# Kernel tuning notes

Hardware: AMD Instinct MI355X
Metric: run time of the kernel (lower is better)

Reference implementation:

```python
import jax, jax.numpy as jnp
import numpy as np

D_MODEL, D_STATE, D_CONV, D_INNER, DT_RANK = 1024, 16, 4, 2048, 64
BATCH, LENGTH = 4, 2048


def setup_inputs() -> dict:
    key = jax.random.key(0)
    ks = jax.random.split(key, 10)
    dt_init_std = DT_RANK ** -0.5
    # dt_proj bias init: inverse-softplus of dt sampled log-uniform in [dt_min, dt_max]
    dt_min, dt_max, dt_floor = 0.001, 0.1, 1e-4
    u = jax.random.uniform(ks[9], (D_INNER,))
    dt = jnp.clip(jnp.exp(u * (np.log(dt_max) - np.log(dt_min)) + np.log(dt_min)), dt_floor, None)
    b_dt = dt + jnp.log(-jnp.expm1(-dt))
    return {
        "x": jax.random.normal(ks[0], (BATCH, LENGTH, D_MODEL), jnp.float32),
        "W_in": jax.random.normal(ks[1], (2 * D_INNER, D_MODEL), jnp.float32) * D_MODEL ** -0.5,
        "conv_w": jax.random.normal(ks[2], (D_INNER, 1, D_CONV), jnp.float32) * D_CONV ** -0.5,
        "conv_b": jax.random.normal(ks[3], (D_INNER,), jnp.float32) * 0.01,
        "W_x": jax.random.normal(ks[4], (DT_RANK + 2 * D_STATE, D_INNER), jnp.float32) * D_INNER ** -0.5,
        "W_dt": jax.random.uniform(ks[5], (D_INNER, DT_RANK), jnp.float32, -dt_init_std, dt_init_std),
        "b_dt": b_dt.astype(jnp.float32),
        "A_raw": jax.random.normal(ks[6], (D_STATE, D_INNER), jnp.float32),
        "D": jax.random.normal(ks[7], (D_INNER,), jnp.float32),
        "W_out": jax.random.normal(ks[8], (D_MODEL, D_INNER), jnp.float32) * D_INNER ** -0.5,
    }


def _mamba_fwd(x, W_in, conv_w, conv_b, W_x, W_dt, b_dt, A_raw, D, W_out):
    b, l, _ = x.shape
    d_inner = W_in.shape[0] // 2
    d_state = A_raw.shape[0]
    dt_rank = W_dt.shape[1]
    xz = jnp.einsum('bld,ed->ble', x, W_in)            # (b, l, 2*d_inner)
    xc, z = jnp.split(xz, 2, axis=-1)
    # causal depthwise conv (torch pads both sides by d_conv-1 then keeps first l == left pad)
    xc = xc.transpose(0, 2, 1)                          # (b, d, l)
    k = conv_w.shape[-1]
    xc = jax.lax.conv_general_dilated(
        xc, conv_w, (1,), [(k - 1, 0)],
        dimension_numbers=('NCH', 'OIH', 'NCH'),
        feature_group_count=d_inner) + conv_b[None, :, None]
    xc = jax.nn.silu(xc).transpose(0, 2, 1)             # (b, l, d)
    dbc = jnp.einsum('bld,ed->ble', xc, W_x)            # (b, l, dt_rank+2*d_state)
    dt, B, C = jnp.split(dbc, [dt_rank, dt_rank + d_state], axis=-1)
    delta = jax.nn.softplus(jnp.einsum('blr,dr->bld', dt, W_dt) + b_dt)  # (b, l, d)
    A = -jnp.exp(A_raw)                                 # (n, d), negative real

    def step(h, inp):
        x_t, dlt, B_t, C_t = inp                        # (b,d),(b,d),(b,n),(b,n)
        dA = jnp.exp(dlt[:, None, :] * A[None])          # (b, n, d)
        h = dA * h + (dlt[:, None, :] * B_t[:, :, None]) * x_t[:, None, :]
        y_t = jnp.einsum('bn,bnd->bd', C_t, h) + D * x_t
        return h, y_t

    h0 = jnp.zeros((b, d_state, d_inner), x.dtype)
    xs = (xc.transpose(1, 0, 2), delta.transpose(1, 0, 2),
          B.transpose(1, 0, 2), C.transpose(1, 0, 2))
    _, ys = jax.lax.scan(step, h0, xs)                  # (l, b, d)
    y = ys.transpose(1, 0, 2) * jax.nn.silu(z)
    return jnp.einsum('bld,md->blm', y, W_out)


def reference(x, W_in, conv_w, conv_b, W_x, W_dt, b_dt, A_raw, D, W_out):
    return _mamba_fwd(x, W_in, conv_w, conv_b, W_x, W_dt, b_dt, A_raw, D, W_out)
```

## Files before the change

### kernel.cpp

```cpp
#include <hip/hip_runtime.h>
#include <hip/hip_bf16.h>

typedef __bf16 bf16;
typedef __bf16 bf16x4 __attribute__((ext_vector_type(4)));
typedef __bf16 bf16x8 __attribute__((ext_vector_type(8)));
typedef float f32x4 __attribute__((ext_vector_type(4)));

__device__ __forceinline__ float fast_exp2(float x) {
#if __has_builtin(__builtin_amdgcn_exp2f)
    return __builtin_amdgcn_exp2f(x);
#else
    return exp2f(x);
#endif
}

__device__ __forceinline__ float fast_log(float x) {
#if __has_builtin(__builtin_amdgcn_logf)
    return __builtin_amdgcn_logf(x) * 0.6931471805599453f;
#else
    return __logf(x);
#endif
}

__device__ __forceinline__ void gload16(bf16* lds, const bf16* g) {
    __builtin_amdgcn_global_load_lds(
        (const __attribute__((address_space(1))) void*)g,
        (__attribute__((address_space(3))) void*)lds,
        16, 0, 0);
}

__device__ __forceinline__ bf16x8 cvt8(const float* p) {
    float4 a = *(const float4*)p;
    float4 b = *(const float4*)(p + 4);
    bf16x8 r;
    r[0] = (bf16)a.x; r[1] = (bf16)a.y; r[2] = (bf16)a.z; r[3] = (bf16)a.w;
    r[4] = (bf16)b.x; r[5] = (bf16)b.y; r[6] = (bf16)b.z; r[7] = (bf16)b.w;
    return r;
}

__global__ __launch_bounds__(256) void cvt_bf16(
    const float* __restrict__ in, bf16* __restrict__ out, int n8)
{
    int i = blockIdx.x * 256 + threadIdx.x;
    if (i < n8)
        *(bf16x8*)(out + (size_t)i * 8) = cvt8(in + (size_t)i * 8);
}

template <int EPI, typename TC>
__global__ __launch_bounds__(256, 2) void gemm_bt(
    const bf16* __restrict__ A, int lda,
    const bf16* __restrict__ B, int ldb,
    TC* __restrict__ C, int ldc,
    int K, int Neff, const float* __restrict__ bias,
    const bf16* __restrict__ gmul, size_t zstride)
{
    __shared__ bf16 As[128 * 32];
    __shared__ bf16 Bs[128 * 32];

    const int tid  = threadIdx.x;
    const int lane = tid & 63;
    const int wave = tid >> 6;
    const int quad = lane >> 4;
    const int l16  = lane & 15;
    const int wm   = (wave >> 1) << 6;
    const int wn   = (wave & 1) << 6;
    const int bm   = blockIdx.x << 7;
    const int bn   = blockIdx.y << 7;
    const int kb   = blockIdx.z * K;

    const int srow = (wave << 4) + (lane >> 2);
    const int scol = (lane & 3) << 3;

    const bf16* Ag0 = A + (size_t)(bm + srow) * lda + kb + scol;
    const bf16* Ag1 = Ag0 + (size_t)lda * 64;
    int br0 = bn + srow;      br0 = br0 < Neff ? br0 : Neff - 1;
    int br1 = bn + srow + 64; br1 = br1 < Neff ? br1 : Neff - 1;
    const bf16* Bg0 = B + (size_t)br0 * ldb + kb + scol;
    const bf16* Bg1 = B + (size_t)br1 * ldb + kb + scol;

    bf16* Asd0 = As + wave * 512;
    bf16* Asd1 = As + wave * 512 + 2048;
    bf16* Bsd0 = Bs + wave * 512;
    bf16* Bsd1 = Bs + wave * 512 + 2048;

    f32x4 acc[4][4] = {};

    for (int k0 = 0; k0 < K; k0 += 32) {
        if (k0) __syncthreads();
        gload16(Asd0, Ag0 + k0);
        gload16(Asd1, Ag1 + k0);
        gload16(Bsd0, Bg0 + k0);
        gload16(Bsd1, Bg1 + k0);
        __syncthreads();

        bf16x8 af[4], bfr[4];
#pragma unroll
        for (int i = 0; i < 4; ++i) {
            af[i]  = *(const bf16x8*)(As + (wm + i * 16 + l16) * 32 + quad * 8);
            bfr[i] = *(const bf16x8*)(Bs + (wn + i * 16 + l16) * 32 + quad * 8);
        }
#pragma unroll
        for (int mi = 0; mi < 4; ++mi)
#pragma unroll
            for (int ni = 0; ni < 4; ++ni)
                acc[mi][ni] = __builtin_amdgcn_mfma_f32_16x16x32_bf16(
                    af[mi], bfr[ni], acc[mi][ni], 0, 0, 0);
    }

    TC* Cz = C + (size_t)blockIdx.z * zstride;

#pragma unroll
    for (int mi = 0; mi < 4; ++mi) {
        const int row = bm + wm + mi * 16 + quad * 4;
#pragma unroll
        for (int ni = 0; ni < 4; ++ni) {
            const int col = bn + wn + ni * 16 + l16;
            if (col < Neff) {
                float bc = (EPI == 1) ? bias[col] : 0.f;
#pragma unroll
                for (int r = 0; r < 4; ++r) {
                    float v = acc[mi][ni][r];
                    if (EPI == 1) {
                        v += bc;
                        float sp = fast_log(1.f + __expf(v));
                        v = (v > 15.f) ? v : sp;
                    } else if (EPI == 2) {
                        float g = v / (1.f + __expf(-v));
                        v = (float)gmul[(size_t)(row + r) * ldc + col] * g;
                    }
                    Cz[(size_t)(row + r) * ldc + col] = (TC)v;
                }
            }
        }
    }
}

__global__ __launch_bounds__(256) void reduce_dbc(
    const float* __restrict__ P, bf16* __restrict__ dbc)
{
    const size_t i = ((size_t)blockIdx.x * 256 + threadIdx.x) * 4;
    f32x4 s = *(const f32x4*)(P + i);
#pragma unroll
    for (int z = 1; z < 4; ++z) {
        f32x4 p = *(const f32x4*)(P + (size_t)z * 786432 + i);
        s[0] += p[0]; s[1] += p[1]; s[2] += p[2]; s[3] += p[3];
    }
    bf16x4 o;
    o[0] = (bf16)s[0]; o[1] = (bf16)s[1]; o[2] = (bf16)s[2]; o[3] = (bf16)s[3];
    *(bf16x4*)(dbc + i) = o;
}

__global__ __launch_bounds__(256) void conv_kernel(
    const bf16* __restrict__ xh, const float* __restrict__ cw,
    const float* __restrict__ cb, bf16* __restrict__ xc)
{
    const int t0 = blockIdx.x << 3;
    const int b  = blockIdx.y;
    const int d  = threadIdx.x * 8;

    float4 wv[8];
#pragma unroll
    for (int i = 0; i < 8; ++i)
        wv[i] = *(const float4*)(cw + (d + i) * 4);

    float4 cb0 = *(const float4*)(cb + d);
    float4 cb1 = *(const float4*)(cb + d + 4);

    float acc[8][8];
#pragma unroll
    for (int k = 0; k < 8; ++k) {
        acc[k][0] = cb0.x; acc[k][1] = cb0.y; acc[k][2] = cb0.z; acc[k][3] = cb0.w;
        acc[k][4] = cb1.x; acc[k][5] = cb1.y; acc[k][6] = cb1.z; acc[k][7] = cb1.w;
    }

    const bf16* base = xh + ((size_t)b * 2048 + t0) * 2048 + d;

#pragma unroll
    for (int r = 0; r < 11; ++r) {
        const int t_in = t0 - 3 + r;
        if (t_in >= 0) {
            bf16x8 v = *(const bf16x8*)(base + (size_t)(r - 3) * 2048);
            float vf[8];
#pragma unroll
            for (int i = 0; i < 8; ++i) vf[i] = (float)v[i];
#pragma unroll
            for (int j = 0; j < 4; ++j) {
                const int local = r - j;
                if (local >= 0 && local < 8) {
#pragma unroll
                    for (int i = 0; i < 8; ++i) {
                        float w = (j == 0) ? wv[i].x : (j == 1) ? wv[i].y
                                : (j == 2) ? wv[i].z : wv[i].w;
                        acc[local][i] += w * vf[i];
                    }
                }
            }
        }
    }

    bf16* ob = xc + ((size_t)b * 2048 + t0) * 2048 + d;
#pragma unroll
    for (int k = 0; k < 8; ++k) {
        bf16x8 o;
#pragma unroll
        for (int i = 0; i < 8; ++i) {
            float s = acc[k][i];
            o[i] = (bf16)(s / (1.f + __expf(-s)));
        }
        *(bf16x8*)(ob + (size_t)k * 2048) = o;
    }
}

__global__ __launch_bounds__(256, 4) void scan_p1(
    const bf16* __restrict__ delta, const bf16* __restrict__ dbc,
    const float* __restrict__ A_raw, const bf16* __restrict__ xc,
    float* __restrict__ Hbuf, bf16* __restrict__ Abuf)
{
    const int d = (blockIdx.x << 8) + threadIdx.x;
    const int b = blockIdx.y;
    const int c = blockIdx.z;

    float A2[16];
#pragma unroll
    for (int n = 0; n < 16; ++n)
        A2[n] = -__expf(A_raw[n * 2048 + d]) * 1.44269504f;

    float h[16];
#pragma unroll
    for (int n = 0; n < 16; ++n) h[n] = 0.f;
    float sdt = 0.f;

    const size_t xbase = ((size_t)(b * 2048 + c * 64)) * 2048 + d;
    const bf16* xp = xc + xbase;
    const bf16* dp = delta + xbase;
    const bf16* bp = dbc + ((size_t)(b * 2048 + c * 64)) * 96 + 64;

    bf16 xr = xp[0], dr = dp[0];
    bf16x8 B0 = *(const bf16x8*)(bp);
    bf16x8 B1 = *(const bf16x8*)(bp + 8);

#pragma unroll 4
    for (int t = 0; t < 64; ++t) {
        const float x  = (float)xr;
        const float dt = (float)dr;
        const bf16x8 Bl = B0, Bh = B1;
        if (t < 63) {
            xr = xp[(size_t)(t + 1) * 2048];
            dr = dp[(size_t)(t + 1) * 2048];
            const bf16* nb = bp + (size_t)(t + 1) * 96;
            B0 = *(const bf16x8*)nb;
            B1 = *(const bf16x8*)(nb + 8);
        }
        const float dx = dt * x;
        sdt += dt;
#pragma unroll
        for (int n = 0; n < 8; ++n) {
            float e = fast_exp2(dt * A2[n]);
            h[n] = e * h[n] + (float)Bl[n] * dx;
        }
#pragma unroll
        for (int n = 0; n < 8; ++n) {
            float e = fast_exp2(dt * A2[n + 8]);
            h[n + 8] = e * h[n + 8] + (float)Bh[n] * dx;
        }
    }

    const size_t hbase = (((size_t)b * 32 + c) * 2048 + d) * 16;
    f32x4* Hp = (f32x4*)(Hbuf + hbase);
#pragma unroll
    for (int r = 0; r < 4; ++r) {
        f32x4 v;
        v[0] = h[r * 4]; v[1] = h[r * 4 + 1];
        v[2] = h[r * 4 + 2]; v[3] = h[r * 4 + 3];
        Hp[r] = v;
    }
    bf16x8 a0, a1;
#pragma unroll
    for (int n = 0; n < 8; ++n) {
        a0[n] = (bf16)fast_exp2(A2[n] * sdt);
        a1[n] = (bf16)fast_exp2(A2[n + 8] * sdt);
    }
    *(bf16x8*)(Abuf + hbase) = a0;
    *(bf16x8*)(Abuf + hbase + 8) = a1;
}

__global__ __launch_bounds__(256) void scan_p2(
    float* __restrict__ Hbuf, const bf16* __restrict__ Abuf)
{
    const int id  = blockIdx.x * 256 + threadIdx.x;
    const int b   = id >> 15;
    const int rem = id & 32767;
    const size_t base = (size_t)b * 32 * 32768 + rem;

    float Hv[32]; bf16 Av[32];
#pragma unroll
    for (int c = 0; c < 32; ++c) {
        Hv[c] = Hbuf[base + (size_t)c * 32768];
        Av[c] = Abuf[base + (size_t)c * 32768];
    }
    float ht = Hv[0];
#pragma unroll
    for (int c = 1; c < 32; ++c) {
        ht = Hv[c] + (float)Av[c] * ht;
        Hbuf[base + (size_t)c * 32768] = ht;
    }
}

__global__ __launch_bounds__(256, 4) void scan_p3(
    const bf16* __restrict__ delta, const bf16* __restrict__ dbc,
    const float* __restrict__ A_raw, const float* __restrict__ Dvec,
    const float* __restrict__ Hbuf, const bf16* xc, bf16* ry)
{
    const int d = (blockIdx.x << 8) + threadIdx.x;
    const int b = blockIdx.y;
    const int c = blockIdx.z;

    float A2[16];
#pragma unroll
    for (int n = 0; n < 16; ++n)
        A2[n] = -__expf(A_raw[n * 2048 + d]) * 1.44269504f;
    const float Dd = Dvec[d];

    float h[16];
    if (c > 0) {
        const f32x4* Hp = (const f32x4*)(
            Hbuf + (((size_t)b * 32 + (c - 1)) * 2048 + d) * 16);
#pragma unroll
        for (int r = 0; r < 4; ++r) {
            f32x4 v = Hp[r];
            h[r * 4] = v[0]; h[r * 4 + 1] = v[1];
            h[r * 4 + 2] = v[2]; h[r * 4 + 3] = v[3];
        }
    } else {
#pragma unroll
        for (int n = 0; n < 16; ++n) h[n] = 0.f;
    }

    const size_t xbase = ((size_t)(b * 2048 + c * 64)) * 2048 + d;
    const bf16* xp = xc + xbase;
    const bf16* dp = delta + xbase;
    const bf16* bp = dbc + ((size_t)(b * 2048 + c * 64)) * 96 + 64;
    bf16* yp = ry + xbase;

    bf16 xr = xp[0], dr = dp[0];
    bf16x8 B0 = *(const bf16x8*)(bp);
    bf16x8 B1 = *(const bf16x8*)(bp + 8);
    bf16x8 C0 = *(const bf16x8*)(bp + 16);
    bf16x8 C1 = *(const bf16x8*)(bp + 24);

#pragma unroll 4
    for (int t = 0; t < 64; ++t) {
        const float x  = (float)xr;
        const float dt = (float)dr;
        const bf16x8 Bl = B0, Bh = B1, Cl = C0, Ch = C1;
        if (t < 63) {
            xr = xp[(size_t)(t + 1) * 2048];
            dr = dp[(size_t)(t + 1) * 2048];
            const bf16* nb = bp + (size_t)(t + 1) * 96;
            B0 = *(const bf16x8*)nb;
            B1 = *(const bf16x8*)(nb + 8);
            C0 = *(const bf16x8*)(nb + 16);
            C1 = *(const bf16x8*)(nb + 24);
        }
        const float dx = dt * x;
        float y = Dd * x;
#pragma unroll
        for (int n = 0; n < 8; ++n) {
            float e = fast_exp2(dt * A2[n]);
            h[n] = e * h[n] + (float)Bl[n] * dx;
            y += (float)Cl[n] * h[n];
        }
#pragma unroll
        for (int n = 0; n < 8; ++n) {
            float e = fast_exp2(dt * A2[n + 8]);
            h[n + 8] = e * h[n + 8] + (float)Bh[n] * dx;
            y += (float)Ch[n] * h[n + 8];
        }
        yp[(size_t)t * 2048] = (bf16)y;
    }
}

extern "C" void kernel_launch(void* const* d_in, const int* in_sizes, int n_in,
                              void* d_out, int out_size, void* d_ws, size_t ws_size,
                              hipStream_t stream)
{
    const float* x      = (const float*)d_in[0];
    const float* W_in   = (const float*)d_in[1];
    const float* conv_w = (const float*)d_in[2];
    const float* conv_b = (const float*)d_in[3];
    const float* W_x    = (const float*)d_in[4];
    const float* W_dt   = (const float*)d_in[5];
    const float* b_dt   = (const float*)d_in[6];
    const float* A_raw  = (const float*)d_in[7];
    const float* Dvec   = (const float*)d_in[8];
    const float* W_out  = (const float*)d_in[9];
    float* out = (float*)d_out;

    char* ws = (char*)d_ws;
    bf16*  buf0   = (bf16*)(ws + 0);
    bf16*  buf1   = (bf16*)(ws + 33554432);
    char*  dob    = (char*)d_out;
    bf16*  dbc    = (bf16*)dob;
    bf16*  xb1    = (bf16*)(dob + 2097152);
    float* Pbuf   = (float*)(dob + 2097152);
    float* Hbuf   = (float*)(dob + 2097152);
    bf16*  xb2    = (bf16*)(dob + 2097152);
    bf16*  Abuf   = (bf16*)(dob + 18874368);
    bf16*  Whi    = (bf16*)(dob + 18874368);
    bf16*  Wxb    = (bf16*)(dob + 27262976);
    bf16*  Wdtb   = (bf16*)(dob + 27787264);
    bf16*  Wlo    = buf1;
    bf16*  Woutb  = buf1;

    cvt_bf16<<<dim3(4096), 256, 0, stream>>>(x, xb1, 1048576);
    cvt_bf16<<<dim3(1024), 256, 0, stream>>>(W_in, Wlo, 262144);
    cvt_bf16<<<dim3(96),   256, 0, stream>>>(W_x, Wxb, 24576);
    cvt_bf16<<<dim3(64),   256, 0, stream>>>(W_dt, Wdtb, 16384);

    gemm_bt<0, bf16><<<dim3(64, 16), 256, 0, stream>>>(
        xb1, 1024, Wlo, 1024, buf0, 2048, 1024, 2048, nullptr, nullptr, 0);
    conv_kernel<<<dim3(256, 4), 256, 0, stream>>>(buf0, conv_w, conv_b, buf1);
    gemm_bt<0, float><<<dim3(64, 1, 4), 256, 0, stream>>>(
        buf1, 2048, Wxb, 2048, Pbuf, 96, 512, 96, nullptr, nullptr, 786432);
    reduce_dbc<<<dim3(768), 256, 0, stream>>>(Pbuf, dbc);
    gemm_bt<1, bf16><<<dim3(64, 16), 256, 0, stream>>>(
        dbc, 96, Wdtb, 64, buf0, 2048, 64, 2048, b_dt, nullptr, 0);
    scan_p1<<<dim3(8, 4, 32), 256, 0, stream>>>(
        buf0, dbc, A_raw, buf1, Hbuf, Abuf);
    scan_p2<<<dim3(512), 256, 0, stream>>>(Hbuf, Abuf);
    scan_p3<<<dim3(8, 4, 32), 256, 0, stream>>>(
        buf0, dbc, A_raw, Dvec, Hbuf, buf1, buf1);
    cvt_bf16<<<dim3(4096), 256, 0, stream>>>(x, xb2, 1048576);
    cvt_bf16<<<dim3(1024), 256, 0, stream>>>(W_in + (size_t)2048 * 1024, Whi, 262144);
    gemm_bt<2, bf16><<<dim3(64, 16), 256, 0, stream>>>(
        xb2, 1024, Whi, 1024, buf0, 2048, 1024, 2048, nullptr, buf1, 0);
    cvt_bf16<<<dim3(1024), 256, 0, stream>>>(W_out, Woutb, 262144);
    gemm_bt<0, float><<<dim3(64, 8), 256, 0, stream>>>(
        buf0, 2048, Woutb, 2048, out, 1024, 2048, 1024, nullptr, nullptr, 0);
}
```

Measured before the change: 427.0 us.

## Use 64 scan chunks with bf16 chunk states and fuse input conversions

The chunked selective scan now splits the sequence into 64 chunks of 32 steps instead of 32 chunks of 64, doubling the blocks in the two per-chunk passes to raise parallelism. Chunk-end states are stored in bf16, and only the per-chunk delta sum is stored; the decay factors are recomputed in the carry pass, which walks all 64 chunks. The separate fp32-to-bf16 conversions of x and the weights, including the upper half of W_in, are merged into one launch. The bf16 carry states reduce accuracy, and the carry pass becomes a longer serial loop with extra exp work.

```diff
diff --git a/kernel.cpp b/kernel.cpp
--- a/kernel.cpp
+++ b/kernel.cpp
@@ -44,6 +44,30 @@
     int i = blockIdx.x * 256 + threadIdx.x;
     if (i < n8)
         *(bf16x8*)(out + (size_t)i * 8) = cvt8(in + (size_t)i * 8);
+}
+
+__global__ __launch_bounds__(256) void cvt_all(
+    const float* __restrict__ x,  const float* __restrict__ W_in,
+    const float* __restrict__ W_x, const float* __restrict__ W_dt,
+    bf16* __restrict__ xb, bf16* __restrict__ Wlo, bf16* __restrict__ Whi,
+    bf16* __restrict__ Wxb, bf16* __restrict__ Wdtb)
+{
+    int i = blockIdx.x * 256 + threadIdx.x;
+    if (i < 1048576) {
+        *(bf16x8*)(xb + (size_t)i * 8) = cvt8(x + (size_t)i * 8);
+    } else if (i < 1310720) {
+        int j = i - 1048576;
+        *(bf16x8*)(Wlo + (size_t)j * 8) = cvt8(W_in + (size_t)j * 8);
+    } else if (i < 1572864) {
+        int j = i - 1310720;
+        *(bf16x8*)(Whi + (size_t)j * 8) = cvt8(W_in + 2097152 + (size_t)j * 8);
+    } else if (i < 1597440) {
+        int j = i - 1572864;
+        *(bf16x8*)(Wxb + (size_t)j * 8) = cvt8(W_x + (size_t)j * 8);
+    } else if (i < 1613824) {
+        int j = i - 1597440;
+        *(bf16x8*)(Wdtb + (size_t)j * 8) = cvt8(W_dt + (size_t)j * 8);
+    }
 }
 
 template <int EPI, typename TC>
@@ -214,7 +238,7 @@
 __global__ __launch_bounds__(256, 4) void scan_p1(
     const bf16* __restrict__ delta, const bf16* __restrict__ dbc,
     const float* __restrict__ A_raw, const bf16* __restrict__ xc,
-    float* __restrict__ Hbuf, bf16* __restrict__ Abuf)
+    bf16* __restrict__ Hb, float* __restrict__ sdtb)
 {
     const int d = (blockIdx.x << 8) + threadIdx.x;
     const int b = blockIdx.y;
@@ -230,21 +254,21 @@
     for (int n = 0; n < 16; ++n) h[n] = 0.f;
     float sdt = 0.f;
 
-    const size_t xbase = ((size_t)(b * 2048 + c * 64)) * 2048 + d;
+    const size_t xbase = ((size_t)(b * 2048 + c * 32)) * 2048 + d;
     const bf16* xp = xc + xbase;
     const bf16* dp = delta + xbase;
-    const bf16* bp = dbc + ((size_t)(b * 2048 + c * 64)) * 96 + 64;
+    const bf16* bp = dbc + ((size_t)(b * 2048 + c * 32)) * 96 + 64;
 
     bf16 xr = xp[0], dr = dp[0];
     bf16x8 B0 = *(const bf16x8*)(bp);
     bf16x8 B1 = *(const bf16x8*)(bp + 8);
 
 #pragma unroll 4
-    for (int t = 0; t < 64; ++t) {
+    for (int t = 0; t < 32; ++t) {
         const float x  = (float)xr;
         const float dt = (float)dr;
         const bf16x8 Bl = B0, Bh = B1;
-        if (t < 63) {
+        if (t < 31) {
             xr = xp[(size_t)(t + 1) * 2048];
             dr = dp[(size_t)(t + 1) * 2048];
             const bf16* nb = bp + (size_t)(t + 1) * 96;
@@ -265,51 +289,46 @@
         }
     }
 
-    const size_t hbase = (((size_t)b * 32 + c) * 2048 + d) * 16;
-    f32x4* Hp = (f32x4*)(Hbuf + hbase);
-#pragma unroll
-    for (int r = 0; r < 4; ++r) {
-        f32x4 v;
-        v[0] = h[r * 4]; v[1] = h[r * 4 + 1];
-        v[2] = h[r * 4 + 2]; v[3] = h[r * 4 + 3];
-        Hp[r] = v;
-    }
-    bf16x8 a0, a1;
+    const size_t hbase = (((size_t)b * 64 + c) * 2048 + d) * 16;
+    bf16x8 h0, h1;
 #pragma unroll
     for (int n = 0; n < 8; ++n) {
-        a0[n] = (bf16)fast_exp2(A2[n] * sdt);
-        a1[n] = (bf16)fast_exp2(A2[n + 8] * sdt);
-    }
-    *(bf16x8*)(Abuf + hbase) = a0;
-    *(bf16x8*)(Abuf + hbase + 8) = a1;
+        h0[n] = (bf16)h[n];
+        h1[n] = (bf16)h[n + 8];
+    }
+    *(bf16x8*)(Hb + hbase) = h0;
+    *(bf16x8*)(Hb + hbase + 8) = h1;
+    sdtb[((size_t)b * 64 + c) * 2048 + d] = sdt;
 }
 
 __global__ __launch_bounds__(256) void scan_p2(
-    float* __restrict__ Hbuf, const bf16* __restrict__ Abuf)
+    bf16* __restrict__ Hb, const float* __restrict__ sdtb,
+    const float* __restrict__ A_raw)
 {
     const int id  = blockIdx.x * 256 + threadIdx.x;
     const int b   = id >> 15;
     const int rem = id & 32767;
-    const size_t base = (size_t)b * 32 * 32768 + rem;
-
-    float Hv[32]; bf16 Av[32];
-#pragma unroll
-    for (int c = 0; c < 32; ++c) {
-        Hv[c] = Hbuf[base + (size_t)c * 32768];
-        Av[c] = Abuf[base + (size_t)c * 32768];
-    }
-    float ht = Hv[0];
-#pragma unroll
-    for (int c = 1; c < 32; ++c) {
-        ht = Hv[c] + (float)Av[c] * ht;
-        Hbuf[base + (size_t)c * 32768] = ht;
+    const int d   = rem >> 4;
+    const int n   = rem & 15;
+
+    const float A2 = -__expf(A_raw[n * 2048 + d]) * 1.44269504f;
+    const size_t hb = (size_t)b * 64 * 32768 + rem;
+    const size_t sb = (size_t)b * 64 * 2048 + d;
+
+    float ht = (float)Hb[hb];
+#pragma unroll 4
+    for (int c = 1; c < 64; ++c) {
+        float Hv = (float)Hb[hb + (size_t)c * 32768];
+        float a  = fast_exp2(A2 * sdtb[sb + (size_t)c * 2048]);
+        ht = Hv + a * ht;
+        Hb[hb + (size_t)c * 32768] = (bf16)ht;
     }
 }
 
 __global__ __launch_bounds__(256, 4) void scan_p3(
     const bf16* __restrict__ delta, const bf16* __restrict__ dbc,
     const float* __restrict__ A_raw, const float* __restrict__ Dvec,
-    const float* __restrict__ Hbuf, const bf16* xc, bf16* ry)
+    const bf16* __restrict__ Hb, const bf16* xc, bf16* ry)
 {
     const int d = (blockIdx.x << 8) + threadIdx.x;
     const int b = blockIdx.y;
@@ -323,23 +342,23 @@
 
     float h[16];
     if (c > 0) {
-        const f32x4* Hp = (const f32x4*)(
-            Hbuf + (((size_t)b * 32 + (c - 1)) * 2048 + d) * 16);
-#pragma unroll
-        for (int r = 0; r < 4; ++r) {
-            f32x4 v = Hp[r];
-            h[r * 4] = v[0]; h[r * 4 + 1] = v[1];
-            h[r * 4 + 2] = v[2]; h[r * 4 + 3] = v[3];
+        const bf16* Hp = Hb + (((size_t)b * 64 + (c - 1)) * 2048 + d) * 16;
+        bf16x8 v0 = *(const bf16x8*)Hp;
+        bf16x8 v1 = *(const bf16x8*)(Hp + 8);
+#pragma unroll
+        for (int n = 0; n < 8; ++n) {
+            h[n]     = (float)v0[n];
+            h[n + 8] = (float)v1[n];
         }
     } else {
 #pragma unroll
         for (int n = 0; n < 16; ++n) h[n] = 0.f;
     }
 
-    const size_t xbase = ((size_t)(b * 2048 + c * 64)) * 2048 + d;
+    const size_t xbase = ((size_t)(b * 2048 + c * 32)) * 2048 + d;
     const bf16* xp = xc + xbase;
     const bf16* dp = delta + xbase;
-    const bf16* bp = dbc + ((size_t)(b * 2048 + c * 64)) * 96 + 64;
+    const bf16* bp = dbc + ((size_t)(b * 2048 + c * 32)) * 96 + 64;
     bf16* yp = ry + xbase;
 
     bf16 xr = xp[0], dr = dp[0];
@@ -349,11 +368,11 @@
     bf16x8 C1 = *(const bf16x8*)(bp + 24);
 
 #pragma unroll 4
-    for (int t = 0; t < 64; ++t) {
+    for (int t = 0; t < 32; ++t) {
         const float x  = (float)xr;
         const float dt = (float)dr;
         const bf16x8 Bl = B0, Bh = B1, Cl = C0, Ch = C1;
-        if (t < 63) {
+        if (t < 31) {
             xr = xp[(size_t)(t + 1) * 2048];
             dr = dp[(size_t)(t + 1) * 2048];
             const bf16* nb = bp + (size_t)(t + 1) * 96;
@@ -403,19 +422,17 @@
     bf16*  dbc    = (bf16*)dob;
     bf16*  xb1    = (bf16*)(dob + 2097152);
     float* Pbuf   = (float*)(dob + 2097152);
-    float* Hbuf   = (float*)(dob + 2097152);
+    bf16*  Hb     = (bf16*)(dob + 2097152);
     bf16*  xb2    = (bf16*)(dob + 2097152);
-    bf16*  Abuf   = (bf16*)(dob + 18874368);
-    bf16*  Whi    = (bf16*)(dob + 18874368);
-    bf16*  Wxb    = (bf16*)(dob + 27262976);
-    bf16*  Wdtb   = (bf16*)(dob + 27787264);
+    float* sdtb   = (float*)(dob + 18874368);
+    bf16*  Whi    = (bf16*)(dob + 20971520);
+    bf16*  Wxb    = (bf16*)(dob + 25165824);
+    bf16*  Wdtb   = (bf16*)(dob + 25690112);
     bf16*  Wlo    = buf1;
     bf16*  Woutb  = buf1;
 
-    cvt_bf16<<<dim3(4096), 256, 0, stream>>>(x, xb1, 1048576);
-    cvt_bf16<<<dim3(1024), 256, 0, stream>>>(W_in, Wlo, 262144);
-    cvt_bf16<<<dim3(96),   256, 0, stream>>>(W_x, Wxb, 24576);
-    cvt_bf16<<<dim3(64),   256, 0, stream>>>(W_dt, Wdtb, 16384);
+    cvt_all<<<dim3(6304), 256, 0, stream>>>(
+        x, W_in, W_x, W_dt, xb1, Wlo, Whi, Wxb, Wdtb);
 
     gemm_bt<0, bf16><<<dim3(64, 16), 256, 0, stream>>>(
         xb1, 1024, Wlo, 1024, buf0, 2048, 1024, 2048, nullptr, nullptr, 0);
@@ -425,13 +442,12 @@
     reduce_dbc<<<dim3(768), 256, 0, stream>>>(Pbuf, dbc);
     gemm_bt<1, bf16><<<dim3(64, 16), 256, 0, stream>>>(
         dbc, 96, Wdtb, 64, buf0, 2048, 64, 2048, b_dt, nullptr, 0);
-    scan_p1<<<dim3(8, 4, 32), 256, 0, stream>>>(
-        buf0, dbc, A_raw, buf1, Hbuf, Abuf);
-    scan_p2<<<dim3(512), 256, 0, stream>>>(Hbuf, Abuf);
-    scan_p3<<<dim3(8, 4, 32), 256, 0, stream>>>(
-        buf0, dbc, A_raw, Dvec, Hbuf, buf1, buf1);
+    scan_p1<<<dim3(8, 4, 64), 256, 0, stream>>>(
+        buf0, dbc, A_raw, buf1, Hb, sdtb);
+    scan_p2<<<dim3(512), 256, 0, stream>>>(Hb, sdtb, A_raw);
+    scan_p3<<<dim3(8, 4, 64), 256, 0, stream>>>(
+        buf0, dbc, A_raw, Dvec, Hb, buf1, buf1);
     cvt_bf16<<<dim3(4096), 256, 0, stream>>>(x, xb2, 1048576);
-    cvt_bf16<<<dim3(1024), 256, 0, stream>>>(W_in + (size_t)2048 * 1024, Whi, 262144);
     gemm_bt<2, bf16><<<dim3(64, 16), 256, 0, stream>>>(
         xb2, 1024, Whi, 1024, buf0, 2048, 1024, 2048, nullptr, buf1, 0);
     cvt_bf16<<<dim3(1024), 256, 0, stream>>>(W_out, Woutb, 262144);
```

After: 417.2 us. 1.02x faster.
